# Kernel tuning notes

Hardware: AMD Instinct MI355X
Metric: run time of the kernel (lower is better)

The kernel has to match this reference:

```python
import jax, jax.numpy as jnp
import numpy as np

HIDDEN = 2048
HEADS = 16
HEAD_DIM = HIDDEN // HEADS
TOP_K = 256
B, N = 1, 2048


def setup_inputs() -> dict:
    key = jax.random.key(0)
    ks = jax.random.split(key, 9)
    s = 0.02
    return {
        "hidden_states": jax.random.normal(ks[0], (B, N, HIDDEN), jnp.float32),
        "Wq": jax.random.normal(ks[1], (HIDDEN, HIDDEN), jnp.float32) * s,
        "bq": jnp.zeros((HIDDEN,), jnp.float32),
        "Wk": jax.random.normal(ks[2], (HIDDEN, HIDDEN), jnp.float32) * s,
        "bk": jnp.zeros((HIDDEN,), jnp.float32),
        "Wv": jax.random.normal(ks[3], (HIDDEN, HIDDEN), jnp.float32) * s,
        "bv": jnp.zeros((HIDDEN,), jnp.float32),
        "Wo": jax.random.normal(ks[4], (HIDDEN, HIDDEN), jnp.float32) * s,
        "bo": jnp.zeros((HIDDEN,), jnp.float32),
    }


def _split_heads(x):
    b, n, _ = x.shape
    return x.reshape(b, n, HEADS, HEAD_DIM).transpose(0, 2, 1, 3)  # b h n d


def reference(hidden_states, Wq, bq, Wk, bk, Wv, bv, Wo, bo):
    scale = 1.0 / jnp.sqrt(jnp.float32(HEAD_DIM))
    q = _split_heads(hidden_states @ Wq + bq)  # [b,h,n,d]
    k = _split_heads(hidden_states @ Wk + bk)
    v = _split_heads(hidden_states @ Wv + bv)

    # Sparse path (kv_seq_length > attention_window): dense QK^T used only to rank keys.
    scores = jnp.einsum("bhnd,bhmd->bhnm", q, k) * scale  # [b,h,n,n]
    importance = scores.mean(axis=2)  # [b,h,n] aggregate over queries
    _, idx = jax.lax.top_k(importance, TOP_K)  # [b,h,k]

    # gather selected K/V (torch.gather along seq dim)
    k_sel = jnp.take_along_axis(k, idx[..., None], axis=2)  # [b,h,k,d]
    v_sel = jnp.take_along_axis(v, idx[..., None], axis=2)

    w = jax.nn.softmax(jnp.einsum("bhnd,bhkd->bhnk", q, k_sel) * scale, axis=-1)
    out = jnp.einsum("bhnk,bhkd->bhnd", w, v_sel)  # [b,h,n,d]
    out = out.transpose(0, 2, 1, 3).reshape(hidden_states.shape[0], -1, HIDDEN)
    return out @ Wo + bo
```

## Files before the change

kernel.cpp:

```cpp
#include <hip/hip_runtime.h>


typedef __attribute__((ext_vector_type(8))) short bf16x8;
typedef __attribute__((ext_vector_type(4))) float f32x4;

__device__ __forceinline__ unsigned short f2bf(float x) {
    unsigned u = __float_as_uint(x);
    u += 0x7fffu + ((u >> 16) & 1u);
    return (unsigned short)(u >> 16);
}

__device__ __forceinline__ void load_lds16(const unsigned short* g, unsigned short* l) {
    __builtin_amdgcn_global_load_lds(
        (const __attribute__((address_space(1))) unsigned int*)g,
        (__attribute__((address_space(3))) unsigned int*)l,
        16, 0, 0);
}

struct Bias3 { const float* p0; const float* p1; const float* p2; };
struct Ptr4  { const float* p[4]; };

template <bool SELECT>
__global__ __launch_bounds__(256) void gemm_bf16(
    const unsigned short* __restrict__ A, long lda, long strideA,
    const unsigned short* __restrict__ Bt, long ldb, long strideB,
    void* __restrict__ Cv, long ldc, long strideC,
    Bias3 bias, int K,
    const int* __restrict__ jpos,
    unsigned short* __restrict__ Ksel,
    unsigned short* __restrict__ VselT)
{
    __shared__ __align__(16) unsigned short As[128][32];
    __shared__ __align__(16) unsigned short Bs[128][32];

    const int tid  = threadIdx.x;
    const int lane = tid & 63;
    const int wave = tid >> 6;
    const int wm = wave >> 1, wn = wave & 1;

    const int bm = blockIdx.y * 128;
    const int bn = blockIdx.x * 128;
    const int b  = blockIdx.z;

    const unsigned short* Ab = A  + (long)b * strideA;
    const unsigned short* Bb = Bt + (long)b * strideB;

    f32x4 acc[4][4];
#pragma unroll
    for (int i = 0; i < 4; i++)
#pragma unroll
        for (int j = 0; j < 4; j++) acc[i][j] = f32x4{0.f, 0.f, 0.f, 0.f};

    const int lr = lane >> 2;
    const int lc = (lane & 3) * 8;

    for (int k0 = 0; k0 < K; k0 += 32) {
        __syncthreads();
#pragma unroll
        for (int r0 = wave * 16; r0 < 128; r0 += 64) {
            load_lds16(Ab + (long)(bm + r0 + lr) * lda + k0 + lc, &As[r0][0]);
            load_lds16(Bb + (long)(bn + r0 + lr) * ldb + k0 + lc, &Bs[r0][0]);
        }
        __syncthreads();

        bf16x8 af[4], bf[4];
#pragma unroll
        for (int s = 0; s < 4; s++)
            af[s] = *(const bf16x8*)&As[wm * 64 + s * 16 + (lane & 15)][(lane >> 4) * 8];
#pragma unroll
        for (int t = 0; t < 4; t++)
            bf[t] = *(const bf16x8*)&Bs[wn * 64 + t * 16 + (lane & 15)][(lane >> 4) * 8];
#pragma unroll
        for (int s = 0; s < 4; s++)
#pragma unroll
            for (int t = 0; t < 4; t++)
                acc[s][t] = __builtin_amdgcn_mfma_f32_16x16x32_bf16(af[s], bf[t], acc[s][t], 0, 0, 0);
    }

    const float* bp = (b == 0) ? bias.p0 : (b == 1) ? bias.p1 : bias.p2;
    float* Cf = (float*)Cv;
    unsigned short* Ch = (unsigned short*)Cv;
#pragma unroll
    for (int s = 0; s < 4; s++) {
#pragma unroll
        for (int t = 0; t < 4; t++) {
            const int col  = bn + wn * 64 + t * 16 + (lane & 15);
            const int row0 = bm + wm * 64 + s * 16 + (lane >> 4) * 4;
#pragma unroll
            for (int r = 0; r < 4; r++) {
                const int row = row0 + r;
                if (SELECT) {
                    const float v = acc[s][t][r] + bp[col];
                    if (b == 0) {
                        Ch[(long)row * ldc + col] = f2bf(v);
                    } else {
                        const int hh = col >> 7, dd = col & 127;
                        const int j = jpos[hh * 2048 + row];
                        if (j >= 0) {
                            if (b == 1) Ksel [hh * 32768 + j * 128 + dd]  = f2bf(v);
                            else        VselT[hh * 32768 + dd * 256 + j]  = f2bf(v);
                        }
                    }
                } else {
                    Cf[(long)b * strideC + (long)row * ldc + col] = acc[s][t][r];
                }
            }
        }
    }
}

__global__ __launch_bounds__(256) void oreduce(const float* __restrict__ part,
                                               const float* __restrict__ bo,
                                               float* __restrict__ out) {
    const long i = ((long)blockIdx.x * 256 + threadIdx.x) * 4;
    float4 a = *(const float4*)(part + i);
    float4 b = *(const float4*)(part + 4194304 + i);
    const int col = (int)(i & 2047);
    float4 o;
    o.x = a.x + b.x + bo[col];
    o.y = a.y + b.y + bo[col + 1];
    o.z = a.z + b.z + bo[col + 2];
    o.w = a.w + b.w + bo[col + 3];
    *(float4*)(out + i) = o;
}

__global__ __launch_bounds__(256, 2) void attn_kernel(
    const unsigned short* __restrict__ Qb,
    const unsigned short* __restrict__ Ksel,
    const unsigned short* __restrict__ VselT,
    unsigned short* __restrict__ Att)
{
    __shared__ __align__(16) unsigned short Qs[64][32];
    __shared__ __align__(16) unsigned short Ks[256][32];
    __shared__ __align__(16) unsigned short Vs[128][32];
    __shared__ __align__(16) unsigned short Ps[64][264];
    __shared__ float linv[64];

    const int tid  = threadIdx.x;
    const int lane = tid & 63;
    const int wave = tid >> 6;
    const int bm = blockIdx.x * 64;
    const int h  = blockIdx.y;
    const int lr = lane >> 2, lc = (lane & 3) * 8;

    const unsigned short* Kh = Ksel  + h * 32768;
    const unsigned short* Vh = VselT + h * 32768;

    f32x4 acc[16];
#pragma unroll
    for (int t = 0; t < 16; t++) acc[t] = f32x4{0.f, 0.f, 0.f, 0.f};

    for (int k0 = 0; k0 < 128; k0 += 32) {
        __syncthreads();
        load_lds16(Qb + (long)(bm + wave * 16 + lr) * 2048 + h * 128 + k0 + lc,
                   &Qs[wave * 16][0]);
#pragma unroll
        for (int q = 0; q < 4; q++)
            load_lds16(Kh + (wave * 64 + q * 16 + lr) * 128 + k0 + lc,
                       &Ks[wave * 64 + q * 16][0]);
        __syncthreads();

        bf16x8 af = *(const bf16x8*)&Qs[wave * 16 + (lane & 15)][(lane >> 4) * 8];
#pragma unroll
        for (int t = 0; t < 16; t++) {
            bf16x8 bfv = *(const bf16x8*)&Ks[t * 16 + (lane & 15)][(lane >> 4) * 8];
            acc[t] = __builtin_amdgcn_mfma_f32_16x16x32_bf16(af, bfv, acc[t], 0, 0, 0);
        }
    }

    const float se = 0.08838834764831845f * 1.4426950408889634f;
#pragma unroll
    for (int r = 0; r < 4; r++) {
        float mx = -3.0e38f;
#pragma unroll
        for (int t = 0; t < 16; t++) mx = fmaxf(mx, acc[t][r]);
#pragma unroll
        for (int off = 1; off < 16; off <<= 1) mx = fmaxf(mx, __shfl_xor(mx, off));
        float sum = 0.f;
#pragma unroll
        for (int t = 0; t < 16; t++) {
            float p = exp2f((acc[t][r] - mx) * se);
            acc[t][r] = p;
            sum += p;
        }
#pragma unroll
        for (int off = 1; off < 16; off <<= 1) sum += __shfl_xor(sum, off);
        const int row = wave * 16 + (lane >> 4) * 4 + r;
#pragma unroll
        for (int t = 0; t < 16; t++)
            Ps[row][t * 16 + (lane & 15)] = f2bf(acc[t][r]);
        if ((lane & 15) == 0) linv[row] = 1.0f / sum;
    }

    const int wm2 = wave >> 1, wn2 = wave & 1;
    f32x4 acc2[2][4];
#pragma unroll
    for (int i = 0; i < 2; i++)
#pragma unroll
        for (int j = 0; j < 4; j++) acc2[i][j] = f32x4{0.f, 0.f, 0.f, 0.f};

    for (int j0 = 0; j0 < 256; j0 += 32) {
        __syncthreads();
#pragma unroll
        for (int q = 0; q < 2; q++)
            load_lds16(Vh + (wave * 32 + q * 16 + lr) * 256 + j0 + lc,
                       &Vs[wave * 32 + q * 16][0]);
        __syncthreads();

        bf16x8 af2[2], bf2v[4];
#pragma unroll
        for (int s2 = 0; s2 < 2; s2++)
            af2[s2] = *(const bf16x8*)&Ps[wm2 * 32 + s2 * 16 + (lane & 15)][j0 + (lane >> 4) * 8];
#pragma unroll
        for (int t2 = 0; t2 < 4; t2++)
            bf2v[t2] = *(const bf16x8*)&Vs[wn2 * 64 + t2 * 16 + (lane & 15)][(lane >> 4) * 8];
#pragma unroll
        for (int s2 = 0; s2 < 2; s2++)
#pragma unroll
            for (int t2 = 0; t2 < 4; t2++)
                acc2[s2][t2] = __builtin_amdgcn_mfma_f32_16x16x32_bf16(af2[s2], bf2v[t2], acc2[s2][t2], 0, 0, 0);
    }

#pragma unroll
    for (int s2 = 0; s2 < 2; s2++) {
#pragma unroll
        for (int t2 = 0; t2 < 4; t2++) {
            const int d = wn2 * 64 + t2 * 16 + (lane & 15);
#pragma unroll
            for (int r = 0; r < 4; r++) {
                const int row = wm2 * 32 + s2 * 16 + (lane >> 4) * 4 + r;
                float v = acc2[s2][t2][r] * linv[row];
                Att[(long)(bm + row) * 2048 + h * 128 + d] = f2bf(v);
            }
        }
    }
}

__global__ __launch_bounds__(256) void prep_kernel(Ptr4 srcs, unsigned short* __restrict__ WT4,
                                                   const float* __restrict__ hs,
                                                   double* __restrict__ part) {
    const int b = blockIdx.x;
    const int tid = threadIdx.x;
    if (b < 16384) {
        __shared__ float tile[32][33];
        const int z = b >> 12, xy = b & 4095;
        const float* W = srcs.p[z];
        unsigned short* WT = WT4 + (long)z * 4194304;
        const int bx = (xy & 63) * 32;
        const int by = (xy >> 6) * 32;
        const int x = tid & 31, y = tid >> 5;
#pragma unroll
        for (int i = 0; i < 32; i += 8)
            tile[y + i][x] = W[(long)(by + y + i) * 2048 + bx + x];
        __syncthreads();
#pragma unroll
        for (int i = 0; i < 32; i += 8)
            WT[(long)(bx + y + i) * 2048 + by + x] = f2bf(tile[x][y + i]);
    } else {
        const int c = b - 16384;
        const int col = (c & 7) * 256 + tid;
        const int r0  = (c >> 3) * 32;
        double a = 0.0;
#pragma unroll 4
        for (int r = 0; r < 32; r++) a += (double)hs[(long)(r0 + r) * 2048 + col];
        part[(long)(c >> 3) * 2048 + col] = a;
    }
}

__global__ void fill_kernel(float* p, float v, long n) {
    long i = ((long)blockIdx.x * blockDim.x + threadIdx.x) * 4;
    if (i + 3 < n) { p[i] = v; p[i+1] = v; p[i+2] = v; p[i+3] = v; }
}

__global__ __launch_bounds__(256) void mean_qsum_part(const double* __restrict__ part,
                                                      const float* __restrict__ Wq,
                                                      double* __restrict__ partq) {
    __shared__ float hsb[32];
    const int j  = blockIdx.x * 256 + threadIdx.x;
    const int i0 = blockIdx.y * 32;
    if (threadIdx.x < 32) {
        double s = 0.0;
#pragma unroll 4
        for (int g = 0; g < 64; g++) s += part[(long)g * 2048 + i0 + threadIdx.x];
        hsb[threadIdx.x] = (float)(s * (1.0 / 2048.0));
    }
    __syncthreads();
    double a = 0.0;
#pragma unroll 4
    for (int r = 0; r < 32; r++)
        a += (double)hsb[r] * (double)Wq[(long)(i0 + r) * 2048 + j];
    partq[(long)blockIdx.y * 2048 + j] = a;
}

__global__ void qsum_fin(const double* __restrict__ partq, const float* __restrict__ bq,
                         float* __restrict__ qbar) {
    const int j = blockIdx.x * 64 + threadIdx.x;
    double s = (double)bq[j];
#pragma unroll 4
    for (int g = 0; g < 64; g++) s += partq[(long)g * 2048 + j];
    qbar[j] = (float)s;
}

__global__ __launch_bounds__(256) void u_kernel(const float* __restrict__ Wk,
                                                const float* __restrict__ qbar,
                                                float* __restrict__ U) {
    const int i = blockIdx.x, t = threadIdx.x;
#pragma unroll
    for (int r = 0; r < 2; r++) {
        const int e = r * 1024 + t * 4;
        float4 w = *(const float4*)(Wk + (long)i * 2048 + e);
        float4 q = *(const float4*)(qbar + e);
        float a = w.x * q.x + w.y * q.y + w.z * q.z + w.w * q.w;
#pragma unroll
        for (int off = 16; off; off >>= 1) a += __shfl_xor(a, off);
        if ((t & 31) == 0) U[(long)i * 16 + r * 8 + (t >> 5)] = a;
    }
}

__global__ __launch_bounds__(256) void cast_imp_kernel(const float* __restrict__ hs,
                                                       const float* __restrict__ U,
                                                       unsigned short* __restrict__ HSb,
                                                       float* __restrict__ imp) {
    __shared__ float row[2048];
    __shared__ float red[4][16];
    const int m = blockIdx.x, t = threadIdx.x;
    for (int i = t; i < 2048; i += 256) {
        float v = hs[(long)m * 2048 + i];
        row[i] = v;
        HSb[(long)m * 2048 + i] = f2bf(v);
    }
    __syncthreads();
    float p[16];
#pragma unroll
    for (int h = 0; h < 16; h++) p[h] = 0.f;
    for (int i = t * 8; i < t * 8 + 8; i++) {
        const float v = row[i];
        const float* u = U + i * 16;
#pragma unroll
        for (int h = 0; h < 16; h++) p[h] += v * u[h];
    }
#pragma unroll
    for (int off = 32; off; off >>= 1)
#pragma unroll
        for (int h = 0; h < 16; h++) p[h] += __shfl_down(p[h], off);
    if ((t & 63) == 0)
#pragma unroll
        for (int h = 0; h < 16; h++) red[t >> 6][h] = p[h];
    __syncthreads();
    if (t < 16)
        imp[(long)t * 2048 + m] = red[0][t] + red[1][t] + red[2][t] + red[3][t];
}

__global__ __launch_bounds__(64) void topk_jpos(const float* __restrict__ imp,
                                                int* __restrict__ jpos) {
    const int h = blockIdx.x;
    const int lane = threadIdx.x;
    unsigned u[32];
#pragma unroll
    for (int r = 0; r < 32; r++) {
        unsigned x = __float_as_uint(imp[(long)h * 2048 + r * 64 + lane]);
        u[r] = (x & 0x80000000u) ? ~x : (x | 0x80000000u);
    }
    unsigned cur = 0;
    for (int b = 31; b >= 0; b--) {
        const unsigned cand = cur | (1u << b);
        int tot = 0;
#pragma unroll
        for (int r = 0; r < 32; r++)
            tot += (int)__popcll(__ballot(u[r] >= cand));
        if (tot >= 256) cur = cand;
    }
    const unsigned long long below = (1ull << lane) - 1ull;
    int pos[32];
    int base = 0;
#pragma unroll
    for (int r = 0; r < 32; r++) {
        const bool q = u[r] > cur;
        const unsigned long long m = __ballot(q);
        pos[r] = q ? base + (int)__popcll(m & below) : -1;
        base += (int)__popcll(m);
    }
#pragma unroll
    for (int r = 0; r < 32; r++) {
        const bool q = (u[r] == cur);
        const unsigned long long m = __ballot(q);
        if (q) {
            const int p = base + (int)__popcll(m & below);
            pos[r] = (p < 256) ? p : -1;
        }
        base += (int)__popcll(m);
    }
#pragma unroll
    for (int r = 0; r < 32; r++)
        jpos[h * 2048 + r * 64 + lane] = pos[r];
}

extern "C" void kernel_launch(void* const* d_in, const int* in_sizes, int n_in,
                              void* d_out, int out_size, void* d_ws, size_t ws_size,
                              hipStream_t stream)
{
    const float* hs = (const float*)d_in[0];
    const float* Wq = (const float*)d_in[1];
    const float* bq = (const float*)d_in[2];
    const float* Wk = (const float*)d_in[3];
    const float* bk = (const float*)d_in[4];
    const float* Wv = (const float*)d_in[5];
    const float* bv = (const float*)d_in[6];
    const float* Wo = (const float*)d_in[7];
    const float* bo = (const float*)d_in[8];

    char* ws = (char*)d_ws;
    size_t off = 0;
    auto alloc = [&](size_t b) -> void* {
        void* p = ws + off;
        off = (off + b + 255) & ~(size_t)255;
        return p;
    };
    unsigned short* HSb   = (unsigned short*)alloc(8388608);
    unsigned short* WT4   = (unsigned short*)alloc(4 * 8388608);
    unsigned short* Qb    = (unsigned short*)alloc(8388608);
    unsigned short* Att   = (unsigned short*)alloc(8388608);
    unsigned short* Ksel  = (unsigned short*)alloc(1048576);
    unsigned short* VselT = (unsigned short*)alloc(1048576);
    float* Opart = (float*)alloc(2 * 16777216);
    double* part  = (double*)alloc(1048576);
    double* partq = (double*)alloc(1048576);
    float* qbar  = (float*)alloc(8192);
    float* U     = (float*)alloc(131072);
    float* imp   = (float*)alloc(131072);
    int*   jpos  = (int*)alloc(131072);

    if (off > ws_size) {
        fill_kernel<<<4096, 256, 0, stream>>>((float*)d_out, 12345.0f, (long)out_size);
        return;
    }

    unsigned short* WoT = WT4 + 3 * 4194304;

    prep_kernel<<<16896, 256, 0, stream>>>(Ptr4{{Wq, Wk, Wv, Wo}}, WT4, hs, part);

    mean_qsum_part<<<dim3(8, 64), 256, 0, stream>>>(part, Wq, partq);
    qsum_fin<<<32, 64, 0, stream>>>(partq, bq, qbar);
    u_kernel<<<2048, 256, 0, stream>>>(Wk, qbar, U);
    cast_imp_kernel<<<2048, 256, 0, stream>>>(hs, U, HSb, imp);

    topk_jpos<<<16, 64, 0, stream>>>(imp, jpos);

    gemm_bf16<true><<<dim3(16, 16, 3), 256, 0, stream>>>(
        HSb, 2048, 0, WT4, 2048, 4194304, Qb, 2048, 0,
        Bias3{bq, bk, bv}, 2048, jpos, Ksel, VselT);

    attn_kernel<<<dim3(32, 16), 256, 0, stream>>>(Qb, Ksel, VselT, Att);

    gemm_bf16<false><<<dim3(16, 16, 2), 256, 0, stream>>>(
        Att, 2048, 1024, WoT, 2048, 1024, Opart, 2048, 4194304,
        Bias3{nullptr, nullptr, nullptr}, 1024, nullptr, nullptr, nullptr);

    oreduce<<<4096, 256, 0, stream>>>(Opart, bo, (float*)d_out);
}
```

Measured before the change: 337.2 us.

## Hoist jpos loads in select epilogue, halve attn barriers, enlarge transpose tiles

The QKV GEMM epilogue now loads the row-to-slot map once per row, outside the column loop, and loads each bias value once per column instead of per element. The attention kernel overlays Q/K/P/V in one shared buffer and stages two 32-wide k-chunks per barrier pair, roughly halving the number of __syncthreads in both matmul phases. The weight transpose/cast kernel switches from 32x32 to 64x64 tiles, so it launches a quarter as many blocks. The bigger shared tile may lower occupancy, and reusing the same buffer for different stages needs the extra barriers to stay correct.

```diff
diff --git a/kernel.cpp b/kernel.cpp
--- a/kernel.cpp
+++ b/kernel.cpp
@@ -80,29 +80,45 @@
     const float* bp = (b == 0) ? bias.p0 : (b == 1) ? bias.p1 : bias.p2;
     float* Cf = (float*)Cv;
     unsigned short* Ch = (unsigned short*)Cv;
-#pragma unroll
-    for (int s = 0; s < 4; s++) {
-#pragma unroll
-        for (int t = 0; t < 4; t++) {
-            const int col  = bn + wn * 64 + t * 16 + (lane & 15);
-            const int row0 = bm + wm * 64 + s * 16 + (lane >> 4) * 4;
-#pragma unroll
-            for (int r = 0; r < 4; r++) {
-                const int row = row0 + r;
-                if (SELECT) {
-                    const float v = acc[s][t][r] + bp[col];
-                    if (b == 0) {
-                        Ch[(long)row * ldc + col] = f2bf(v);
-                    } else {
-                        const int hh = col >> 7, dd = col & 127;
-                        const int j = jpos[hh * 2048 + row];
-                        if (j >= 0) {
-                            if (b == 1) Ksel [hh * 32768 + j * 128 + dd]  = f2bf(v);
-                            else        VselT[hh * 32768 + dd * 256 + j]  = f2bf(v);
-                        }
+
+    if (SELECT && b != 0) {
+        const int hh = bn >> 7;
+        int jv[4][4];
+#pragma unroll
+        for (int s = 0; s < 4; s++)
+#pragma unroll
+            for (int r = 0; r < 4; r++)
+                jv[s][r] = jpos[hh * 2048 + bm + wm * 64 + s * 16 + (lane >> 4) * 4 + r];
+#pragma unroll
+        for (int s = 0; s < 4; s++) {
+#pragma unroll
+            for (int t = 0; t < 4; t++) {
+                const int col = bn + wn * 64 + t * 16 + (lane & 15);
+                const int dd  = col & 127;
+                const float bv = bp[col];
+#pragma unroll
+                for (int r = 0; r < 4; r++) {
+                    const int j = jv[s][r];
+                    if (j >= 0) {
+                        const unsigned short h16 = f2bf(acc[s][t][r] + bv);
+                        if (b == 1) Ksel [hh * 32768 + j * 128 + dd] = h16;
+                        else        VselT[hh * 32768 + dd * 256 + j] = h16;
                     }
-                } else {
-                    Cf[(long)b * strideC + (long)row * ldc + col] = acc[s][t][r];
+                }
+            }
+        }
+    } else {
+#pragma unroll
+        for (int s = 0; s < 4; s++) {
+#pragma unroll
+            for (int t = 0; t < 4; t++) {
+                const int col  = bn + wn * 64 + t * 16 + (lane & 15);
+                const int row0 = bm + wm * 64 + s * 16 + (lane >> 4) * 4;
+#pragma unroll
+                for (int r = 0; r < 4; r++) {
+                    const int row = row0 + r;
+                    if (SELECT) Ch[(long)row * ldc + col] = f2bf(acc[s][t][r] + bp[col]);
+                    else        Cf[(long)b * strideC + (long)row * ldc + col] = acc[s][t][r];
                 }
             }
         }
@@ -124,16 +140,18 @@
     *(float4*)(out + i) = o;
 }
 
+#define QS_OFF(c)  ((c) * 2048)
+#define KS_OFF(c)  (4096 + (c) * 8192)
+#define PS_OFF     0
+#define VS_OFF(c)  (16896 + (c) * 4096)
+
 __global__ __launch_bounds__(256, 2) void attn_kernel(
     const unsigned short* __restrict__ Qb,
     const unsigned short* __restrict__ Ksel,
     const unsigned short* __restrict__ VselT,
     unsigned short* __restrict__ Att)
 {
-    __shared__ __align__(16) unsigned short Qs[64][32];
-    __shared__ __align__(16) unsigned short Ks[256][32];
-    __shared__ __align__(16) unsigned short Vs[128][32];
-    __shared__ __align__(16) unsigned short Ps[64][264];
+    __shared__ __align__(16) unsigned short smem[25088];
     __shared__ float linv[64];
 
     const int tid  = threadIdx.x;
@@ -150,23 +168,31 @@
 #pragma unroll
     for (int t = 0; t < 16; t++) acc[t] = f32x4{0.f, 0.f, 0.f, 0.f};
 
-    for (int k0 = 0; k0 < 128; k0 += 32) {
-        __syncthreads();
-        load_lds16(Qb + (long)(bm + wave * 16 + lr) * 2048 + h * 128 + k0 + lc,
-                   &Qs[wave * 16][0]);
-#pragma unroll
-        for (int q = 0; q < 4; q++)
-            load_lds16(Kh + (wave * 64 + q * 16 + lr) * 128 + k0 + lc,
-                       &Ks[wave * 64 + q * 16][0]);
-        __syncthreads();
-
-        bf16x8 af = *(const bf16x8*)&Qs[wave * 16 + (lane & 15)][(lane >> 4) * 8];
-#pragma unroll
-        for (int t = 0; t < 16; t++) {
-            bf16x8 bfv = *(const bf16x8*)&Ks[t * 16 + (lane & 15)][(lane >> 4) * 8];
-            acc[t] = __builtin_amdgcn_mfma_f32_16x16x32_bf16(af, bfv, acc[t], 0, 0, 0);
-        }
-    }
+#pragma unroll
+    for (int c2 = 0; c2 < 2; c2++) {
+        __syncthreads();
+#pragma unroll
+        for (int c = 0; c < 2; c++) {
+            const int k0 = c2 * 64 + c * 32;
+            load_lds16(Qb + (long)(bm + wave * 16 + lr) * 2048 + h * 128 + k0 + lc,
+                       &smem[QS_OFF(c) + wave * 512]);
+#pragma unroll
+            for (int q = 0; q < 4; q++)
+                load_lds16(Kh + (wave * 64 + q * 16 + lr) * 128 + k0 + lc,
+                           &smem[KS_OFF(c) + (wave * 64 + q * 16) * 32]);
+        }
+        __syncthreads();
+#pragma unroll
+        for (int kk = 0; kk < 2; kk++) {
+            bf16x8 af = *(const bf16x8*)&smem[QS_OFF(kk) + (wave * 16 + (lane & 15)) * 32 + (lane >> 4) * 8];
+#pragma unroll
+            for (int t = 0; t < 16; t++) {
+                bf16x8 bfv = *(const bf16x8*)&smem[KS_OFF(kk) + (t * 16 + (lane & 15)) * 32 + (lane >> 4) * 8];
+                acc[t] = __builtin_amdgcn_mfma_f32_16x16x32_bf16(af, bfv, acc[t], 0, 0, 0);
+            }
+        }
+    }
+    __syncthreads();
 
     const float se = 0.08838834764831845f * 1.4426950408889634f;
 #pragma unroll
@@ -188,7 +214,7 @@
         const int row = wave * 16 + (lane >> 4) * 4 + r;
 #pragma unroll
         for (int t = 0; t < 16; t++)
-            Ps[row][t * 16 + (lane & 15)] = f2bf(acc[t][r]);
+            smem[PS_OFF + row * 264 + t * 16 + (lane & 15)] = f2bf(acc[t][r]);
         if ((lane & 15) == 0) linv[row] = 1.0f / sum;
     }
 
@@ -199,26 +225,34 @@
 #pragma unroll
         for (int j = 0; j < 4; j++) acc2[i][j] = f32x4{0.f, 0.f, 0.f, 0.f};
 
-    for (int j0 = 0; j0 < 256; j0 += 32) {
-        __syncthreads();
-#pragma unroll
-        for (int q = 0; q < 2; q++)
-            load_lds16(Vh + (wave * 32 + q * 16 + lr) * 256 + j0 + lc,
-                       &Vs[wave * 32 + q * 16][0]);
-        __syncthreads();
-
-        bf16x8 af2[2], bf2v[4];
-#pragma unroll
-        for (int s2 = 0; s2 < 2; s2++)
-            af2[s2] = *(const bf16x8*)&Ps[wm2 * 32 + s2 * 16 + (lane & 15)][j0 + (lane >> 4) * 8];
-#pragma unroll
-        for (int t2 = 0; t2 < 4; t2++)
-            bf2v[t2] = *(const bf16x8*)&Vs[wn2 * 64 + t2 * 16 + (lane & 15)][(lane >> 4) * 8];
-#pragma unroll
-        for (int s2 = 0; s2 < 2; s2++)
+#pragma unroll
+    for (int c2 = 0; c2 < 4; c2++) {
+#pragma unroll
+        for (int c = 0; c < 2; c++) {
+            const int j0 = c2 * 64 + c * 32;
+#pragma unroll
+            for (int q = 0; q < 2; q++)
+                load_lds16(Vh + (wave * 32 + q * 16 + lr) * 256 + j0 + lc,
+                           &smem[VS_OFF(c) + (wave * 32 + q * 16) * 32]);
+        }
+        __syncthreads();
+#pragma unroll
+        for (int c = 0; c < 2; c++) {
+            const int j0 = c2 * 64 + c * 32;
+            bf16x8 af2[2], bf2v[4];
+#pragma unroll
+            for (int s2 = 0; s2 < 2; s2++)
+                af2[s2] = *(const bf16x8*)&smem[PS_OFF + (wm2 * 32 + s2 * 16 + (lane & 15)) * 264 + j0 + (lane >> 4) * 8];
 #pragma unroll
             for (int t2 = 0; t2 < 4; t2++)
-                acc2[s2][t2] = __builtin_amdgcn_mfma_f32_16x16x32_bf16(af2[s2], bf2v[t2], acc2[s2][t2], 0, 0, 0);
+                bf2v[t2] = *(const bf16x8*)&smem[VS_OFF(c) + (wn2 * 64 + t2 * 16 + (lane & 15)) * 32 + (lane >> 4) * 8];
+#pragma unroll
+            for (int s2 = 0; s2 < 2; s2++)
+#pragma unroll
+                for (int t2 = 0; t2 < 4; t2++)
+                    acc2[s2][t2] = __builtin_amdgcn_mfma_f32_16x16x32_bf16(af2[s2], bf2v[t2], acc2[s2][t2], 0, 0, 0);
+        }
+        __syncthreads();
     }
 
 #pragma unroll
@@ -241,23 +275,23 @@
                                                    double* __restrict__ part) {
     const int b = blockIdx.x;
     const int tid = threadIdx.x;
-    if (b < 16384) {
-        __shared__ float tile[32][33];
-        const int z = b >> 12, xy = b & 4095;
+    if (b < 4096) {
+        __shared__ float tile[64][65];
+        const int z = b >> 10, xy = b & 1023;
         const float* W = srcs.p[z];
         unsigned short* WT = WT4 + (long)z * 4194304;
-        const int bx = (xy & 63) * 32;
-        const int by = (xy >> 6) * 32;
-        const int x = tid & 31, y = tid >> 5;
-#pragma unroll
-        for (int i = 0; i < 32; i += 8)
+        const int bx = (xy & 31) * 64;
+        const int by = (xy >> 5) * 64;
+        const int x = tid & 63, y = tid >> 6;
+#pragma unroll
+        for (int i = 0; i < 64; i += 4)
             tile[y + i][x] = W[(long)(by + y + i) * 2048 + bx + x];
         __syncthreads();
 #pragma unroll
-        for (int i = 0; i < 32; i += 8)
+        for (int i = 0; i < 64; i += 4)
             WT[(long)(bx + y + i) * 2048 + by + x] = f2bf(tile[x][y + i]);
     } else {
-        const int c = b - 16384;
+        const int c = b - 4096;
         const int col = (c & 7) * 256 + tid;
         const int r0  = (c >> 3) * 32;
         double a = 0.0;
@@ -437,7 +471,7 @@
 
     unsigned short* WoT = WT4 + 3 * 4194304;
 
-    prep_kernel<<<16896, 256, 0, stream>>>(Ptr4{{Wq, Wk, Wv, Wo}}, WT4, hs, part);
+    prep_kernel<<<4608, 256, 0, stream>>>(Ptr4{{Wq, Wk, Wv, Wo}}, WT4, hs, part);
 
     mean_qsum_part<<<dim3(8, 64), 256, 0, stream>>>(part, Wq, partq);
     qsum_fin<<<32, 64, 0, stream>>>(partq, bq, qbar);
```

Result: faster. 327.0 us (-3.0%).
